# Performance work log

Hardware: AMD Instinct MI355X
Metric: run time of the kernel (lower is better)

## Reference

```python
import jax, jax.numpy as jnp
import numpy as np

HEADS = 12
DIM_HEAD = 64
SCALE = DIM_HEAD ** -0.5


def rotate_every_two(x):
    # (..., 2d) -> rotate pairs: (x1, x2) -> (-x2, x1)
    x = x.reshape(*x.shape[:-1], -1, 2)
    x1, x2 = x[..., 0], x[..., 1]
    return jnp.stack((-x2, x1), axis=-1).reshape(*x.shape[:-2], -1)


def apply_rotary_pos_emb(q, k, sinu_pos):
    # sinu_pos: (b, p, 2c) -> sin, cos each (b, p, c)
    b, p, two_c = sinu_pos.shape
    sp = sinu_pos.reshape(b, p, 2, two_c // 2)
    sin, cos = sp[:, :, 0, :], sp[:, :, 1, :]
    # interleave-repeat to (b, 1, p, 2c) to broadcast over heads
    sin = jnp.repeat(sin, 2, axis=-1)[:, None, :, :]
    cos = jnp.repeat(cos, 2, axis=-1)[:, None, :, :]
    rot = lambda t: t * cos + rotate_every_two(t) * sin
    return rot(q), rot(k)


def setup_inputs() -> dict:
    key = jax.random.key(0)
    ks = jax.random.split(key, 5)
    b, n, dim = 8, 1024, 768
    inner = HEADS * DIM_HEAD
    x = jax.random.normal(ks[0], (b, n, dim), dtype=jnp.float32)
    pos_emb = jax.random.normal(ks[1], (1, n, DIM_HEAD), dtype=jnp.float32)
    W_qkv = jax.random.normal(ks[2], (dim, 3 * inner), dtype=jnp.float32) * (dim ** -0.5)
    W_out = jax.random.normal(ks[3], (inner, dim), dtype=jnp.float32) * (inner ** -0.5)
    b_out = jnp.zeros((dim,), dtype=jnp.float32)
    return {"x": x, "pos_emb": pos_emb, "W_qkv": W_qkv, "W_out": W_out, "b_out": b_out}


def reference(x, pos_emb, W_qkv, W_out, b_out):
    b, n, _ = x.shape
    qkv = x @ W_qkv                                   # (b, n, 3*inner)
    q, k, v = jnp.split(qkv, 3, axis=-1)
    split_heads = lambda t: t.reshape(b, n, HEADS, DIM_HEAD).transpose(0, 2, 1, 3)
    q, k, v = split_heads(q), split_heads(k), split_heads(v)   # (b, h, n, d)
    q, k = apply_rotary_pos_emb(q, k, pos_emb)
    dots = jnp.einsum('bhid,bhjd->bhij', q, k) * SCALE
    attn = jax.nn.softmax(dots, axis=-1)
    out = jnp.einsum('bhij,bhjd->bhid', attn, v)
    out = out.transpose(0, 2, 1, 3).reshape(b, n, HEADS * DIM_HEAD)
    out = out @ W_out + b_out
    return out  # context is None -> torch code returns (out[:, :n], None); n == full length
```

## Files before the change

### kernel.cpp

```cpp
#include <hip/hip_runtime.h>
#include <hip/hip_bf16.h>

typedef __attribute__((ext_vector_type(8))) short bf16x8;
typedef __attribute__((ext_vector_type(4))) float f32x4;
typedef __attribute__((ext_vector_type(4))) unsigned short u16x4;
typedef unsigned short u16;
typedef unsigned int u32;

#define DEVINL __device__ __forceinline__

DEVINL u16 f2bf(float f) {
    union { float f; u32 u; } v; v.f = f;
    u32 r = v.u + 0x7FFFu + ((v.u >> 16) & 1u);
    return (u16)(r >> 16);
}
DEVINL float bf2f(u16 h) {
    union { u32 u; float f; } v; v.u = ((u32)h) << 16;
    return v.f;
}
DEVINL u32 cvt_pk_bf16(float lo, float hi) {
    u32 r;
    asm("v_cvt_pk_bf16_f32 %0, %1, %2" : "=v"(r) : "v"(lo), "v"(hi));
    return r;
}

template<int Nv> DEVINL void vmcnt_asm() {
    if constexpr (Nv == 0) asm volatile("s_waitcnt vmcnt(0)" ::: "memory");
    else if constexpr (Nv == 3) asm volatile("s_waitcnt vmcnt(3)" ::: "memory");
    else if constexpr (Nv == 5) asm volatile("s_waitcnt vmcnt(5)" ::: "memory");
    else if constexpr (Nv == 6) asm volatile("s_waitcnt vmcnt(6)" ::: "memory");
    else if constexpr (Nv == 7) asm volatile("s_waitcnt vmcnt(7)" ::: "memory");
    else asm volatile("s_waitcnt vmcnt(4)" ::: "memory");
}

#define GLOAD_LDS16(g, l) __builtin_amdgcn_global_load_lds( \
    (const __attribute__((address_space(1))) void*)(g), \
    (__attribute__((address_space(3))) void*)(l), 16, 0, 0)

#define SBAR() do { \
    __builtin_amdgcn_sched_barrier(0); \
    __builtin_amdgcn_s_barrier(); \
    __builtin_amdgcn_sched_barrier(0); } while (0)

__global__ __launch_bounds__(256) void prep_kernel(const float* __restrict__ x,
                                                   u16* __restrict__ xb,
                                                   const float* __restrict__ W_qkv,
                                                   u16* __restrict__ Wqkv_t,
                                                   const float* __restrict__ W_out,
                                                   u16* __restrict__ Wout_t) {
    __shared__ float tile[32][33];
    const int bid = blockIdx.x;
    if (bid < 3072) {
        int t = bid * 256 + threadIdx.x;
        const float4 v0 = reinterpret_cast<const float4*>(x)[t * 2];
        const float4 v1 = reinterpret_cast<const float4*>(x)[t * 2 + 1];
        u16 o[8];
        o[0] = f2bf(v0.x); o[1] = f2bf(v0.y); o[2] = f2bf(v0.z); o[3] = f2bf(v0.w);
        o[4] = f2bf(v1.x); o[5] = f2bf(v1.y); o[6] = f2bf(v1.z); o[7] = f2bf(v1.w);
        *reinterpret_cast<bf16x8*>(xb + (size_t)t * 8) = *reinterpret_cast<bf16x8*>(o);
        return;
    }
    const float* in; u16* out; int R, C, bx, by;
    if (bid < 4800) {
        int u = bid - 3072; in = W_qkv; out = Wqkv_t; R = 768; C = 2304;
        bx = u % 72; by = u / 72;
    } else {
        int u = bid - 4800; in = W_out; out = Wout_t; R = 768; C = 768;
        bx = u % 24; by = u / 24;
    }
    int c0 = bx * 32, r0 = by * 32;
    int tx = threadIdx.x & 31, ty = threadIdx.x >> 5;
#pragma unroll
    for (int i = 0; i < 4; ++i)
        tile[ty + i * 8][tx] = in[(size_t)(r0 + ty + i * 8) * C + c0 + tx];
    __syncthreads();
#pragma unroll
    for (int i = 0; i < 4; ++i)
        out[(size_t)(c0 + ty + i * 8) * R + r0 + tx] = f2bf(tile[tx][ty + i * 8]);
}

template<int K>
__global__ __launch_bounds__(256, 3) void gemm1_kernel(const u16* __restrict__ A,
                                                       const u16* __restrict__ Bt,
                                                       u16* __restrict__ Cout) {
    constexpr int NT = K / 32;
    constexpr int PBUF = (128 + 192) * 32;
    __shared__ u16 lds[2 * PBUF];

    const int tid = threadIdx.x;
    const int wv = tid >> 6, lane = tid & 63;
    const int lr = lane & 15, lg = lane >> 4;
    const int wr = wv >> 1, wc = wv & 1;

    const int id = blockIdx.x;
    const int sid = (id & 7) * 96 + (id >> 3);
    const int bm = (sid / 12) * 128;
    const int bn = (sid % 12) * 192;

#define STAGE(nb_, kt_) do { \
    _Pragma("unroll") \
    for (int j_ = 0; j_ < 2; ++j_) { \
        const int idx_ = j_ * 256 + tid; \
        const int row_ = idx_ >> 2; \
        const int c_ = (idx_ & 3) ^ ((row_ >> 1) & 3); \
        GLOAD_LDS16(A + (size_t)(bm + row_) * K + (kt_) * 32 + c_ * 8, \
                    (char*)lds + (nb_) * (PBUF * 2) + j_ * 4096 + tid * 16); \
    } \
    _Pragma("unroll") \
    for (int j_ = 0; j_ < 3; ++j_) { \
        const int idx_ = j_ * 256 + tid; \
        const int row_ = idx_ >> 2; \
        const int c_ = (idx_ & 3) ^ ((row_ >> 1) & 3); \
        GLOAD_LDS16(Bt + (size_t)(bn + row_) * K + (kt_) * 32 + c_ * 8, \
                    (char*)lds + (nb_) * (PBUF * 2) + 8192 + j_ * 4096 + tid * 16); \
    } } while (0)

    f32x4 acc[4][6];
#pragma unroll
    for (int i = 0; i < 4; ++i)
#pragma unroll
        for (int j = 0; j < 6; ++j) acc[i][j] = (f32x4){0.f, 0.f, 0.f, 0.f};

    STAGE(0, 0);
    __builtin_amdgcn_sched_barrier(0);
    vmcnt_asm<0>();
    SBAR();

    for (int kt = 0; kt < NT; ++kt) {
        const int cur = kt & 1;
        if (kt < NT - 1) {
            STAGE(cur ^ 1, kt + 1);
            __builtin_amdgcn_sched_barrier(0);
            vmcnt_asm<5>();
            SBAR();
        } else {
            __builtin_amdgcn_sched_barrier(0);
            vmcnt_asm<0>();
            SBAR();
        }
        bf16x8 af[4], bfr[6];
#pragma unroll
        for (int mf = 0; mf < 4; ++mf) {
            const int row = wr * 64 + mf * 16 + lr;
            af[mf] = *reinterpret_cast<const bf16x8*>(
                &lds[cur * PBUF + row * 32 + ((lg ^ ((row >> 1) & 3)) << 3)]);
        }
#pragma unroll
        for (int nf = 0; nf < 6; ++nf) {
            const int row = wc * 96 + nf * 16 + lr;
            bfr[nf] = *reinterpret_cast<const bf16x8*>(
                &lds[cur * PBUF + 4096 + row * 32 + ((lg ^ ((row >> 1) & 3)) << 3)]);
        }
        __builtin_amdgcn_s_setprio(1);
#pragma unroll
        for (int mf = 0; mf < 4; ++mf)
#pragma unroll
            for (int nf = 0; nf < 6; ++nf)
                acc[mf][nf] = __builtin_amdgcn_mfma_f32_16x16x32_bf16(
                    af[mf], bfr[nf], acc[mf][nf], 0, 0, 0);
        __builtin_amdgcn_s_setprio(0);
        SBAR();
    }

#pragma unroll
    for (int mf = 0; mf < 4; ++mf)
#pragma unroll
        for (int nf = 0; nf < 6; ++nf) {
            const int col = bn + wc * 96 + nf * 16 + lr;
#pragma unroll
            for (int r = 0; r < 4; ++r) {
                const int row = bm + wr * 64 + mf * 16 + lg * 4 + r;
                Cout[(size_t)row * 2304 + col] = f2bf(acc[mf][nf][r]);
            }
        }
#undef STAGE
}

template<int NTN, int NFRAG, int BROWS, int K, bool BF16_OUT>
__global__ __launch_bounds__(512, 2) void gemm_bigtile_kernel(const u16* __restrict__ A,
                                                              const u16* __restrict__ Bt,
                                                              void* __restrict__ Cout,
                                                              const float* __restrict__ bias) {
    constexpr int BN = NFRAG * 32;
    constexpr int N = NTN * BN;
    constexpr int NT = K / 64;
    constexpr int PA = 256 * 32;
    constexpr int PB = BROWS * 32;
    constexpr int PKS = PA + PB;
    constexpr int PBUF = 2 * PKS;
    constexpr int BFULL = (BROWS * 4) / 512;
    constexpr int BREM = (BROWS * 4) % 512;
    __shared__ u16 lds[2 * PBUF];

    const int tid = threadIdx.x;
    const int wv = tid >> 6, lane = tid & 63;
    const int lr = lane & 15, lg = lane >> 4;
    const int wr = wv >> 1, wc = wv & 1;

    const int id = blockIdx.x;
    const int sid = (id & 7) * 32 + (id >> 3);
    const int bm = (sid / NTN) * 256;
    const int bn = (sid % NTN) * BN;

#define PL(buf_, ks_, mat_) ((buf_) * PBUF + (ks_) * PKS + (mat_) * PA)

#define STAGE_A(nb_, kt_, ks_) do { \
    _Pragma("unroll") \
    for (int j_ = 0; j_ < 2; ++j_) { \
        const int idx_ = j_ * 512 + tid; \
        const int row_ = idx_ >> 2; \
        const int c_ = (idx_ & 3) ^ ((row_ >> 1) & 3); \
        GLOAD_LDS16(A + (size_t)(bm + row_) * K + (kt_) * 64 + (ks_) * 32 + c_ * 8, \
                    (char*)lds + PL((nb_), (ks_), 0) * 2 + j_ * 8192 + tid * 16); \
    } } while (0)

#define STAGE_B(nb_, kt_, ks_) do { \
    _Pragma("unroll") \
    for (int j_ = 0; j_ < BFULL; ++j_) { \
        const int idx_ = j_ * 512 + tid; \
        const int row_ = idx_ >> 2; \
        const int c_ = (idx_ & 3) ^ ((row_ >> 1) & 3); \
        GLOAD_LDS16(Bt + (size_t)(bn + row_) * K + (kt_) * 64 + (ks_) * 32 + c_ * 8, \
                    (char*)lds + PL((nb_), (ks_), 1) * 2 + j_ * 8192 + tid * 16); \
    } \
    if constexpr (BREM != 0) { \
        if (tid < BREM) { \
            const int idx_ = BFULL * 512 + tid; \
            const int row_ = idx_ >> 2; \
            const int c_ = (idx_ & 3) ^ ((row_ >> 1) & 3); \
            GLOAD_LDS16(Bt + (size_t)(bn + row_) * K + (kt_) * 64 + (ks_) * 32 + c_ * 8, \
                        (char*)lds + PL((nb_), (ks_), 1) * 2 + BFULL * 8192 + tid * 16); \
        } \
    } } while (0)

#define LDA(mh_, ks_, cur_) do { \
    _Pragma("unroll") \
    for (int f_ = 0; f_ < 2; ++f_) { \
        const int row_ = wr * 64 + (mh_) * 32 + f_ * 16 + lr; \
        af[f_] = *reinterpret_cast<const bf16x8*>( \
            &lds[PL((cur_), (ks_), 0) + row_ * 32 + ((lg ^ ((row_ >> 1) & 3)) << 3)]); \
    } } while (0)

#define LDB(ks_, cur_) do { \
    _Pragma("unroll") \
    for (int nf_ = 0; nf_ < NFRAG; ++nf_) { \
        const int row_ = wc * (NFRAG * 16) + nf_ * 16 + lr; \
        bfr[nf_] = *reinterpret_cast<const bf16x8*>( \
            &lds[PL((cur_), (ks_), 1) + row_ * 32 + ((lg ^ ((row_ >> 1) & 3)) << 3)]); \
    } } while (0)

#define MFMAQ(mh_) do { \
    __builtin_amdgcn_s_setprio(1); \
    _Pragma("unroll") \
    for (int f_ = 0; f_ < 2; ++f_) \
    _Pragma("unroll") \
    for (int nf_ = 0; nf_ < NFRAG; ++nf_) \
        acc[(mh_) * 2 + f_][nf_] = __builtin_amdgcn_mfma_f32_16x16x32_bf16( \
            af[f_], bfr[nf_], acc[(mh_) * 2 + f_][nf_], 0, 0, 0); \
    __builtin_amdgcn_s_setprio(0); } while (0)

#define WAITHALF() do { \
    __builtin_amdgcn_sched_barrier(0); \
    if constexpr (BREM != 0) { \
        if (wv < BREM / 64) vmcnt_asm<2 + BFULL + 1>(); \
        else vmcnt_asm<2 + BFULL>(); \
    } else { \
        vmcnt_asm<2 + BFULL>(); \
    } } while (0)

    f32x4 acc[4][NFRAG];
#pragma unroll
    for (int i = 0; i < 4; ++i)
#pragma unroll
        for (int j = 0; j < NFRAG; ++j) acc[i][j] = (f32x4){0.f, 0.f, 0.f, 0.f};

    bf16x8 af[2], bfr[NFRAG];

    STAGE_A(0, 0, 0); STAGE_B(0, 0, 0); STAGE_A(0, 0, 1); STAGE_B(0, 0, 1);
    __builtin_amdgcn_sched_barrier(0);
    vmcnt_asm<0>();
    SBAR();

    for (int kt = 0; kt < NT - 1; ++kt) {
        const int cur = kt & 1, nxt = cur ^ 1;
        LDB(0, cur); LDA(0, 0, cur);
        STAGE_A(nxt, kt + 1, 0);
        SBAR(); MFMAQ(0); SBAR();
        LDA(1, 0, cur);
        STAGE_B(nxt, kt + 1, 0);
        WAITHALF();
        SBAR(); MFMAQ(1); SBAR();
        LDB(1, cur); LDA(0, 1, cur);
        STAGE_A(nxt, kt + 1, 1);
        SBAR(); MFMAQ(0); SBAR();
        LDA(1, 1, cur);
        STAGE_B(nxt, kt + 1, 1);
        WAITHALF();
        SBAR(); MFMAQ(1); SBAR();
    }
    {
        const int cur = (NT - 1) & 1;
        LDB(0, cur); LDA(0, 0, cur); SBAR(); MFMAQ(0); SBAR();
        LDA(1, 0, cur);
        __builtin_amdgcn_sched_barrier(0);
        vmcnt_asm<0>();
        SBAR(); MFMAQ(1); SBAR();
        LDB(1, cur); LDA(0, 1, cur); SBAR(); MFMAQ(0); SBAR();
        LDA(1, 1, cur); SBAR(); MFMAQ(1);
    }

#pragma unroll
    for (int mf = 0; mf < 4; ++mf)
#pragma unroll
        for (int nf = 0; nf < NFRAG; ++nf) {
            const int col = bn + wc * (NFRAG * 16) + nf * 16 + lr;
            const float bv = BF16_OUT ? 0.f : bias[col];
#pragma unroll
            for (int r = 0; r < 4; ++r) {
                const int row = bm + wr * 64 + mf * 16 + lg * 4 + r;
                if (BF16_OUT)
                    ((u16*)Cout)[(size_t)row * N + col] = f2bf(acc[mf][nf][r]);
                else
                    ((float*)Cout)[(size_t)row * N + col] = acc[mf][nf][r] + bv;
            }
        }
#undef PL
#undef STAGE_A
#undef STAGE_B
#undef LDA
#undef LDB
#undef MFMAQ
#undef WAITHALF
}

__global__ __launch_bounds__(256) void rot_vtrans_kernel(u16* __restrict__ qkv,
                                                         const float* __restrict__ pos,
                                                         u16* __restrict__ Vt) {
    __shared__ u16 tile[64][72];
    const int bid = blockIdx.x;
    if (bid < 6144) {
        int t = bid * 256 + threadIdx.x;
        int row = t / 192;
        int col = (t % 192) * 8;
        int n = row & 1023;
        int i0 = (col & 63) >> 1;
        const float qs = (col < 768) ? 0.18033688f : 1.0f;
        const float* pn = pos + (size_t)n * 64;
        u16* p = qkv + (size_t)row * 2304 + col;
        bf16x8 v = *reinterpret_cast<bf16x8*>(p);
        u16 o[8];
#pragma unroll
        for (int j = 0; j < 4; ++j) {
            float s = pn[i0 + j], c = pn[32 + i0 + j];
            float x0 = bf2f((u16)v[2 * j]), x1 = bf2f((u16)v[2 * j + 1]);
            o[2 * j]     = f2bf((x0 * c - x1 * s) * qs);
            o[2 * j + 1] = f2bf((x1 * c + x0 * s) * qs);
        }
        *reinterpret_cast<bf16x8*>(p) = *reinterpret_cast<bf16x8*>(o);
    } else {
        int u = bid - 6144;
        int nt = u & 15;
        int bh = u >> 4;
        int b = bh / 12, h = bh % 12;
        int tid = threadIdx.x;
        int rr = tid >> 3, cc = (tid & 7) * 8;
#pragma unroll
        for (int it = 0; it < 2; ++it) {
            int nloc = it * 32 + rr;
            const u16* src = qkv + (size_t)(b * 1024 + nt * 64 + nloc) * 2304 + 1536 + h * 64 + cc;
            bf16x8 v = *reinterpret_cast<const bf16x8*>(src);
#pragma unroll
            for (int j = 0; j < 8; ++j) tile[nloc][cc + j] = (u16)v[j];
        }
        __syncthreads();
#pragma unroll
        for (int it = 0; it < 2; ++it) {
            int d = it * 32 + rr;
            u16 o[8];
#pragma unroll
            for (int j = 0; j < 8; ++j) o[j] = tile[cc + j][d];
            *reinterpret_cast<bf16x8*>(Vt + (size_t)(bh * 64 + d) * 1024 + nt * 64 + cc) =
                *reinterpret_cast<bf16x8*>(o);
        }
    }
}

__global__ __launch_bounds__(512, 8) void attn_kernel(const u16* __restrict__ qkv,
                                                      const u16* __restrict__ Vt,
                                                      u16* __restrict__ attn_out) {
    __shared__ u16 Ks[2][64 * 64];
    __shared__ u16 Vs[2][64 * 64];
    const int d_ = blockIdx.x;
    const int bh = ((d_ >> 3) >> 3) * 8 + (d_ & 7);
    const int qt = (d_ >> 3) & 7;
    const int b = bh / 12, h = bh % 12;
    const int tid = threadIdx.x;
    const int w = tid >> 6, lr = tid & 15, lg = (tid >> 4) & 3;

    bf16x8 qf[2];
#pragma unroll
    for (int ds = 0; ds < 2; ++ds)
        qf[ds] = *reinterpret_cast<const bf16x8*>(
            &qkv[(size_t)(b * 1024 + qt * 128 + w * 16 + lr) * 2304 + h * 64 + ds * 32 + lg * 8]);

    f32x4 o[4];
#pragma unroll
    for (int i = 0; i < 4; ++i) o[i] = (f32x4){0.f, 0.f, 0.f, 0.f};
    float lsum = 0.f;

    const int srow = tid >> 3;
    const int scol = ((tid & 7) ^ (srow & 7)) * 8;
    const int srowK = (srow & 0x20) | ((srow & 0x0C) << 1) | ((srow & 0x10) >> 2) | (srow & 3);

#define STAGE_KV(nb, kt_) do { \
    GLOAD_LDS16(qkv + (size_t)(b * 1024 + (kt_) * 64 + srowK) * 2304 + 768 + h * 64 + scol, \
                (char*)Ks[nb] + tid * 16); \
    GLOAD_LDS16(Vt + (size_t)(bh * 64 + srow) * 1024 + (kt_) * 64 + scol, \
                (char*)Vs[nb] + tid * 16); \
} while (0)

    STAGE_KV(0, 0);
    __syncthreads();

    const int rsw = lr & 7;

    for (int kt = 0; kt < 16; ++kt) {
        const int cur = kt & 1;
        if (kt < 15) STAGE_KV(cur ^ 1, kt + 1);

        f32x4 s[4];
        __builtin_amdgcn_s_setprio(1);
#pragma unroll
        for (int kf = 0; kf < 4; ++kf) {
            f32x4 acc = (f32x4){0.f, 0.f, 0.f, 0.f};
#pragma unroll
            for (int ds = 0; ds < 2; ++ds) {
                bf16x8 kfr = *reinterpret_cast<const bf16x8*>(
                    &Ks[cur][(kf * 16 + lr) * 64 + (((ds * 4 + lg) ^ rsw) * 8)]);
                acc = __builtin_amdgcn_mfma_f32_16x16x32_bf16(kfr, qf[ds], acc, 0, 0, 0);
            }
            s[kf] = acc;
        }
        __builtin_amdgcn_s_setprio(0);

#pragma unroll
        for (int kf = 0; kf < 4; ++kf)
#pragma unroll
            for (int r = 0; r < 4; ++r) s[kf][r] = __builtin_amdgcn_exp2f(s[kf][r]);
        {
            float t0 = (s[0][0] + s[0][1]) + (s[0][2] + s[0][3]);
            float t1 = (s[1][0] + s[1][1]) + (s[1][2] + s[1][3]);
            float t2 = (s[2][0] + s[2][1]) + (s[2][2] + s[2][3]);
            float t3 = (s[3][0] + s[3][1]) + (s[3][2] + s[3][3]);
            lsum += (t0 + t1) + (t2 + t3);
        }

        union { u32 wd[4]; bf16x8 v; } pk[2];
#pragma unroll
        for (int ks = 0; ks < 2; ++ks) {
            pk[ks].wd[0] = cvt_pk_bf16(s[2 * ks][0], s[2 * ks][1]);
            pk[ks].wd[1] = cvt_pk_bf16(s[2 * ks][2], s[2 * ks][3]);
            pk[ks].wd[2] = cvt_pk_bf16(s[2 * ks + 1][0], s[2 * ks + 1][1]);
            pk[ks].wd[3] = cvt_pk_bf16(s[2 * ks + 1][2], s[2 * ks + 1][3]);
        }

        __builtin_amdgcn_s_setprio(1);
#pragma unroll
        for (int ks = 0; ks < 2; ++ks) {
#pragma unroll
            for (int df = 0; df < 4; ++df) {
                bf16x8 vb = *reinterpret_cast<const bf16x8*>(
                    &Vs[cur][(df * 16 + lr) * 64 + (((ks * 4 + lg) ^ rsw) * 8)]);
                o[df] = __builtin_amdgcn_mfma_f32_16x16x32_bf16(vb, pk[ks].v, o[df], 0, 0, 0);
            }
        }
        __builtin_amdgcn_s_setprio(0);
        __syncthreads();
    }
#undef STAGE_KV

    lsum += __shfl_xor(lsum, 16);
    lsum += __shfl_xor(lsum, 32);
    const float linv = 1.0f / lsum;

    u16* orow = attn_out + (size_t)(b * 1024 + qt * 128 + w * 16 + lr) * 768 + h * 64 + lg * 4;
#pragma unroll
    for (int df = 0; df < 4; ++df) {
        uint2 st;
        st.x = cvt_pk_bf16(o[df][0] * linv, o[df][1] * linv);
        st.y = cvt_pk_bf16(o[df][2] * linv, o[df][3] * linv);
        *reinterpret_cast<uint2*>(orow + df * 16) = st;
    }
}

extern "C" void kernel_launch(void* const* d_in, const int* in_sizes, int n_in,
                              void* d_out, int out_size, void* d_ws, size_t ws_size,
                              hipStream_t stream) {
    (void)in_sizes; (void)n_in; (void)out_size; (void)ws_size;
    const float* x     = (const float*)d_in[0];
    const float* pos   = (const float*)d_in[1];
    const float* W_qkv = (const float*)d_in[2];
    const float* W_out = (const float*)d_in[3];
    const float* b_out = (const float*)d_in[4];
    float* out = (float*)d_out;

    char* ws = (char*)d_ws;
    u16* xb     = (u16*)(ws);
    u16* Wqkv_t = (u16*)(ws + 12582912);
    u16* Wout_t = (u16*)(ws + 16171008);
    u16* qkv    = (u16*)(ws + 17399808);
    u16* Vt     = (u16*)(ws + 55148544);
    u16* attn_o = (u16*)(ws + 67731456);

    prep_kernel<<<5376, 256, 0, stream>>>(x, xb, W_qkv, Wqkv_t, W_out, Wout_t);
    gemm1_kernel<768><<<768, 256, 0, stream>>>(xb, Wqkv_t, qkv);
    rot_vtrans_kernel<<<7680, 256, 0, stream>>>(qkv, pos, Vt);
    attn_kernel<<<768, 512, 0, stream>>>(qkv, Vt, attn_o);
    gemm_bigtile_kernel<8, 3, 128, 768, false><<<256, 512, 0, stream>>>(attn_o, Wout_t, out, b_out);
}
```

Baseline: 113.7 us.

## Process two query sub-tiles per wave in attention to reuse K/V LDS fragments

The attention kernel now uses 256 threads (4 waves) per block instead of 512, and each wave handles 32 query rows as two 16-row sub-tiles. Each K and V fragment read from LDS feeds two MFMAs, which halves LDS read traffic per unit of work, and each thread issues two global-to-LDS loads per stage. The cost is more registers per thread (doubled accumulators and score arrays) and fewer waves per block to hide latency. The launch bounds change to (256,3) to match.

```diff
diff --git a/kernel.cpp b/kernel.cpp
--- a/kernel.cpp
+++ b/kernel.cpp
@@ -385,7 +385,7 @@
     }
 }
 
-__global__ __launch_bounds__(512, 8) void attn_kernel(const u16* __restrict__ qkv,
+__global__ __launch_bounds__(256, 3) void attn_kernel(const u16* __restrict__ qkv,
                                                       const u16* __restrict__ Vt,
                                                       u16* __restrict__ attn_out) {
     __shared__ u16 Ks[2][64 * 64];
@@ -397,27 +397,34 @@
     const int tid = threadIdx.x;
     const int w = tid >> 6, lr = tid & 15, lg = (tid >> 4) & 3;
 
-    bf16x8 qf[2];
-#pragma unroll
-    for (int ds = 0; ds < 2; ++ds)
-        qf[ds] = *reinterpret_cast<const bf16x8*>(
-            &qkv[(size_t)(b * 1024 + qt * 128 + w * 16 + lr) * 2304 + h * 64 + ds * 32 + lg * 8]);
-
-    f32x4 o[4];
-#pragma unroll
-    for (int i = 0; i < 4; ++i) o[i] = (f32x4){0.f, 0.f, 0.f, 0.f};
-    float lsum = 0.f;
-
-    const int srow = tid >> 3;
-    const int scol = ((tid & 7) ^ (srow & 7)) * 8;
-    const int srowK = (srow & 0x20) | ((srow & 0x0C) << 1) | ((srow & 0x10) >> 2) | (srow & 3);
+    bf16x8 qf[2][2];
+#pragma unroll
+    for (int q = 0; q < 2; ++q)
+#pragma unroll
+        for (int ds = 0; ds < 2; ++ds)
+            qf[q][ds] = *reinterpret_cast<const bf16x8*>(
+                &qkv[(size_t)(b * 1024 + qt * 128 + w * 32 + q * 16 + lr) * 2304 +
+                     h * 64 + ds * 32 + lg * 8]);
+
+    f32x4 o[2][4];
+#pragma unroll
+    for (int q = 0; q < 2; ++q)
+#pragma unroll
+        for (int i = 0; i < 4; ++i) o[q][i] = (f32x4){0.f, 0.f, 0.f, 0.f};
+    float lsum[2] = {0.f, 0.f};
 
 #define STAGE_KV(nb, kt_) do { \
-    GLOAD_LDS16(qkv + (size_t)(b * 1024 + (kt_) * 64 + srowK) * 2304 + 768 + h * 64 + scol, \
-                (char*)Ks[nb] + tid * 16); \
-    GLOAD_LDS16(Vt + (size_t)(bh * 64 + srow) * 1024 + (kt_) * 64 + scol, \
-                (char*)Vs[nb] + tid * 16); \
-} while (0)
+    _Pragma("unroll") \
+    for (int j_ = 0; j_ < 2; ++j_) { \
+        const int idx_ = j_ * 256 + tid; \
+        const int row_ = idx_ >> 3; \
+        const int sc_ = ((idx_ & 7) ^ (row_ & 7)) * 8; \
+        const int rk_ = (row_ & 0x20) | ((row_ & 0x0C) << 1) | ((row_ & 0x10) >> 2) | (row_ & 3); \
+        GLOAD_LDS16(qkv + (size_t)(b * 1024 + (kt_) * 64 + rk_) * 2304 + 768 + h * 64 + sc_, \
+                    (char*)Ks[nb] + idx_ * 16); \
+        GLOAD_LDS16(Vt + (size_t)(bh * 64 + row_) * 1024 + (kt_) * 64 + sc_, \
+                    (char*)Vs[nb] + idx_ * 16); \
+    } } while (0)
 
     STAGE_KV(0, 0);
     __syncthreads();
@@ -428,40 +435,42 @@
         const int cur = kt & 1;
         if (kt < 15) STAGE_KV(cur ^ 1, kt + 1);
 
-        f32x4 s[4];
+        f32x4 s[2][4];
         __builtin_amdgcn_s_setprio(1);
 #pragma unroll
         for (int kf = 0; kf < 4; ++kf) {
-            f32x4 acc = (f32x4){0.f, 0.f, 0.f, 0.f};
-#pragma unroll
-            for (int ds = 0; ds < 2; ++ds) {
-                bf16x8 kfr = *reinterpret_cast<const bf16x8*>(
-                    &Ks[cur][(kf * 16 + lr) * 64 + (((ds * 4 + lg) ^ rsw) * 8)]);
-                acc = __builtin_amdgcn_mfma_f32_16x16x32_bf16(kfr, qf[ds], acc, 0, 0, 0);
+            bf16x8 k0 = *reinterpret_cast<const bf16x8*>(
+                &Ks[cur][(kf * 16 + lr) * 64 + ((lg ^ rsw) * 8)]);
+            bf16x8 k1 = *reinterpret_cast<const bf16x8*>(
+                &Ks[cur][(kf * 16 + lr) * 64 + (((4 + lg) ^ rsw) * 8)]);
+#pragma unroll
+            for (int q = 0; q < 2; ++q) {
+                f32x4 a = __builtin_amdgcn_mfma_f32_16x16x32_bf16(
+                    k0, qf[q][0], (f32x4){0.f, 0.f, 0.f, 0.f}, 0, 0, 0);
+                s[q][kf] = __builtin_amdgcn_mfma_f32_16x16x32_bf16(k1, qf[q][1], a, 0, 0, 0);
             }
-            s[kf] = acc;
         }
         __builtin_amdgcn_s_setprio(0);
 
-#pragma unroll
-        for (int kf = 0; kf < 4; ++kf)
-#pragma unroll
-            for (int r = 0; r < 4; ++r) s[kf][r] = __builtin_amdgcn_exp2f(s[kf][r]);
-        {
-            float t0 = (s[0][0] + s[0][1]) + (s[0][2] + s[0][3]);
-            float t1 = (s[1][0] + s[1][1]) + (s[1][2] + s[1][3]);
-            float t2 = (s[2][0] + s[2][1]) + (s[2][2] + s[2][3]);
-            float t3 = (s[3][0] + s[3][1]) + (s[3][2] + s[3][3]);
-            lsum += (t0 + t1) + (t2 + t3);
-        }
-
-        union { u32 wd[4]; bf16x8 v; } pk[2];
-#pragma unroll
-        for (int ks = 0; ks < 2; ++ks) {
-            pk[ks].wd[0] = cvt_pk_bf16(s[2 * ks][0], s[2 * ks][1]);
-            pk[ks].wd[1] = cvt_pk_bf16(s[2 * ks][2], s[2 * ks][3]);
-            pk[ks].wd[2] = cvt_pk_bf16(s[2 * ks + 1][0], s[2 * ks + 1][1]);
-            pk[ks].wd[3] = cvt_pk_bf16(s[2 * ks + 1][2], s[2 * ks + 1][3]);
+        union { u32 wd[4]; bf16x8 v; } pk[2][2];
+#pragma unroll
+        for (int q = 0; q < 2; ++q) {
+#pragma unroll
+            for (int kf = 0; kf < 4; ++kf)
+#pragma unroll
+                for (int r = 0; r < 4; ++r) s[q][kf][r] = __builtin_amdgcn_exp2f(s[q][kf][r]);
+            float t0 = (s[q][0][0] + s[q][0][1]) + (s[q][0][2] + s[q][0][3]);
+            float t1 = (s[q][1][0] + s[q][1][1]) + (s[q][1][2] + s[q][1][3]);
+            float t2 = (s[q][2][0] + s[q][2][1]) + (s[q][2][2] + s[q][2][3]);
+            float t3 = (s[q][3][0] + s[q][3][1]) + (s[q][3][2] + s[q][3][3]);
+            lsum[q] += (t0 + t1) + (t2 + t3);
+#pragma unroll
+            for (int ks = 0; ks < 2; ++ks) {
+                pk[q][ks].wd[0] = cvt_pk_bf16(s[q][2 * ks][0], s[q][2 * ks][1]);
+                pk[q][ks].wd[1] = cvt_pk_bf16(s[q][2 * ks][2], s[q][2 * ks][3]);
+                pk[q][ks].wd[2] = cvt_pk_bf16(s[q][2 * ks + 1][0], s[q][2 * ks + 1][1]);
+                pk[q][ks].wd[3] = cvt_pk_bf16(s[q][2 * ks + 1][2], s[q][2 * ks + 1][3]);
+            }
         }
 
         __builtin_amdgcn_s_setprio(1);
@@ -471,7 +480,8 @@
             for (int df = 0; df < 4; ++df) {
                 bf16x8 vb = *reinterpret_cast<const bf16x8*>(
                     &Vs[cur][(df * 16 + lr) * 64 + (((ks * 4 + lg) ^ rsw) * 8)]);
-                o[df] = __builtin_amdgcn_mfma_f32_16x16x32_bf16(vb, pk[ks].v, o[df], 0, 0, 0);
+                o[0][df] = __builtin_amdgcn_mfma_f32_16x16x32_bf16(vb, pk[0][ks].v, o[0][df], 0, 0, 0);
+                o[1][df] = __builtin_amdgcn_mfma_f32_16x16x32_bf16(vb, pk[1][ks].v, o[1][df], 0, 0, 0);
             }
         }
         __builtin_amdgcn_s_setprio(0);
@@ -479,17 +489,21 @@
     }
 #undef STAGE_KV
 
-    lsum += __shfl_xor(lsum, 16);
-    lsum += __shfl_xor(lsum, 32);
-    const float linv = 1.0f / lsum;
-
-    u16* orow = attn_out + (size_t)(b * 1024 + qt * 128 + w * 16 + lr) * 768 + h * 64 + lg * 4;
-#pragma unroll
-    for (int df = 0; df < 4; ++df) {
-        uint2 st;
-        st.x = cvt_pk_bf16(o[df][0] * linv, o[df][1] * linv);
-        st.y = cvt_pk_bf16(o[df][2] * linv, o[df][3] * linv);
-        *reinterpret_cast<uint2*>(orow + df * 16) = st;
+#pragma unroll
+    for (int q = 0; q < 2; ++q) {
+        float l = lsum[q];
+        l += __shfl_xor(l, 16);
+        l += __shfl_xor(l, 32);
+        const float linv = 1.0f / l;
+        u16* orow = attn_out +
+            (size_t)(b * 1024 + qt * 128 + w * 32 + q * 16 + lr) * 768 + h * 64 + lg * 4;
+#pragma unroll
+        for (int df = 0; df < 4; ++df) {
+            uint2 st;
+            st.x = cvt_pk_bf16(o[q][df][0] * linv, o[q][df][1] * linv);
+            st.y = cvt_pk_bf16(o[q][df][2] * linv, o[q][df][3] * linv);
+            *reinterpret_cast<uint2*>(orow + df * 16) = st;
+        }
     }
 }
 
@@ -515,6 +529,6 @@
     prep_kernel<<<5376, 256, 0, stream>>>(x, xb, W_qkv, Wqkv_t, W_out, Wout_t);
     gemm1_kernel<768><<<768, 256, 0, stream>>>(xb, Wqkv_t, qkv);
     rot_vtrans_kernel<<<7680, 256, 0, stream>>>(qkv, pos, Vt);
-    attn_kernel<<<768, 512, 0, stream>>>(qkv, Vt, attn_o);
+    attn_kernel<<<768, 256, 0, stream>>>(qkv, Vt, attn_o);
     gemm_bigtile_kernel<8, 3, 128, 768, false><<<256, 512, 0, stream>>>(attn_o, Wout_t, out, b_out);
 }
```

Result: faster. 109.2 us (-3.9%).
